# Performance work log

Hardware: AMD Instinct MI355X
Metric: run time of the kernel (lower is better)

Reference implementation:

```python
import jax, jax.numpy as jnp
import numpy as np

N_NODES = 100000
N_EDGES = 1200000
N_GRAPHS = 1024
IN_FEATS = 64
HID = 64
BN_EPS = 1e-5


def setup_inputs() -> dict:
    key = jax.random.key(0)
    ks = jax.random.split(key, 20)
    feats = jax.random.normal(ks[0], (N_NODES, IN_FEATS), jnp.float32)
    src = jax.random.randint(ks[1], (N_EDGES,), 0, N_NODES, jnp.int32)
    dst = jax.random.randint(ks[2], (N_EDGES,), 0, N_NODES, jnp.int32)
    graph_ids = jnp.sort(jax.random.randint(ks[3], (N_NODES,), 0, N_GRAPHS, jnp.int32))

    def lin(k, fi, fo):
        s = 1.0 / np.sqrt(fi)
        kw, kb = jax.random.split(k)
        return (jax.random.uniform(kw, (fi, fo), jnp.float32, -s, s),
                jax.random.uniform(kb, (fo,), jnp.float32, -s, s))

    W_self, _ = lin(ks[4], IN_FEATS, HID)
    W_neigh, b_neigh = lin(ks[5], IN_FEATS, HID)
    W1, b1 = lin(ks[6], HID, 128)
    W2, b2 = lin(ks[7], 128, 64)
    W3, b3 = lin(ks[8], 64, 1)

    def bn(k, d):
        k1, k2, k3, k4 = jax.random.split(k, 4)
        return (jax.random.normal(k1, (d,), jnp.float32) * 0.1 + 1.0,
                jax.random.normal(k2, (d,), jnp.float32) * 0.1,
                jax.random.normal(k3, (d,), jnp.float32) * 0.1,
                jax.random.uniform(k4, (d,), jnp.float32, 0.5, 1.5))

    g1, be1, rm1, rv1 = bn(ks[9], 128)
    g2, be2, rm2, rv2 = bn(ks[10], 64)

    return dict(feats=feats, src=src, dst=dst, graph_ids=graph_ids,
                W_self=W_self, W_neigh=W_neigh, b_neigh=b_neigh,
                W1=W1, b1=b1, g1=g1, be1=be1, rm1=rm1, rv1=rv1,
                W2=W2, b2=b2, g2=g2, be2=be2, rm2=rm2, rv2=rv2,
                W3=W3, b3=b3)


def reference(feats, src, dst, graph_ids, W_self, W_neigh, b_neigh,
              W1, b1, g1, be1, rm1, rv1, W2, b2, g2, be2, rm2, rv2, W3, b3):
    # --- SAGEConv (mean aggregator): h = W_self@h_self + W_neigh@mean_neigh + b
    deg = jax.ops.segment_sum(jnp.ones((src.shape[0],), feats.dtype), dst,
                              num_segments=N_NODES)                      # [N]
    agg = jax.ops.segment_sum(feats[src], dst, num_segments=N_NODES)     # [N, F]
    mean_neigh = agg / jnp.maximum(deg, 1.0)[:, None]
    h = feats @ W_self + mean_neigh @ W_neigh + b_neigh
    h = jax.nn.relu(h)                                                   # activation

    # --- per-graph max readout (dgl.max_nodes)
    hg = jax.ops.segment_max(h, graph_ids, num_segments=N_GRAPHS)        # [G, HID]

    # --- MLP head with eval-mode BatchNorm1d
    def bn(x, g, b, rm, rv):
        return (x - rm) * jax.lax.rsqrt(rv + BN_EPS) * g + b

    x = bn(jax.nn.relu(hg @ W1 + b1), g1, be1, rm1, rv1)
    x = bn(jax.nn.relu(x @ W2 + b2), g2, be2, rm2, rv2)
    return x @ W3 + b3                                                   # [G, n_task]
```

## Files before the change

### kernel.cpp

```cpp
#include <hip/hip_runtime.h>
#include <hip/hip_fp16.h>

#define N_NODES  100000
#define N_EDGES  1200000
#define N_GRAPHS 1024
#define F        64
#define BN_EPS   1e-5f
#define NBUCK    ((N_NODES + 255) / 256)
#define NBLK     512
#define CHUNK    ((N_EDGES + NBLK - 1) / NBLK)
#define MT       128
#define GEMM_BLOCKS ((N_NODES + MT - 1) / MT)
#define CE       3584
#define LDA      72

typedef _Float16 f16x8 __attribute__((ext_vector_type(8)));
typedef float f32x4 __attribute__((ext_vector_type(4)));

__global__ __launch_bounds__(256) void prep(
    const float* __restrict__ feats, const float* __restrict__ Wself,
    const float* __restrict__ Wneigh, __half* __restrict__ Uh,
    __half* __restrict__ Zh, const int* __restrict__ dst,
    int* __restrict__ bcnt, int* __restrict__ hgbits) {
  __shared__ __align__(16) char smraw[2 * 128 * LDA * 2];
  int t = threadIdx.x;

  if (blockIdx.x >= GEMM_BLOCKS) {
    int* lh = (int*)smraw;
    int b = blockIdx.x - GEMM_BLOCKS;
    int zidx = b * 256 + t;
    if (zidx < N_GRAPHS * F) hgbits[zidx] = 0;
    for (int i = t; i < NBUCK; i += 256) lh[i] = 0;
    __syncthreads();
    int e0 = b * CHUNK, e1 = e0 + CHUNK;
    if (e1 > N_EDGES) e1 = N_EDGES;
    for (int e = e0 + t; e < e1; e += 256) atomicAdd(&lh[dst[e] >> 8], 1);
    __syncthreads();
    for (int i = t; i < NBUCK; i += 256) {
      int c = lh[i];
      if (c) atomicAdd(&bcnt[i], c);
    }
    return;
  }

  __half* As = (__half*)smraw;
  __half* Bs = As + 128 * LDA;
  int mbase = blockIdx.x * MT;

#pragma unroll
  for (int s = 0; s < 8; s++) {
    int idx = s * 256 + t;
    int row = idx >> 4, c4 = idx & 15;
    int gm = mbase + row;
    float4 v = (gm < N_NODES) ? *(const float4*)(feats + (size_t)gm * F + c4 * 4)
                              : make_float4(0.f, 0.f, 0.f, 0.f);
    union { __half h[4]; uint2 u; } pk;
    pk.h[0] = __float2half_rn(v.x); pk.h[1] = __float2half_rn(v.y);
    pk.h[2] = __float2half_rn(v.z); pk.h[3] = __float2half_rn(v.w);
    *(uint2*)(As + row * LDA + c4 * 4) = pk.u;
  }

#pragma unroll
  for (int s = 0; s < 2; s++) {
    int unit = s * 256 + t;
    int kq = unit >> 5, c4 = unit & 31;
    const float* Wp = (c4 < 16) ? (Wself + c4 * 4) : (Wneigh + (c4 - 16) * 4);
    float4 w0 = *(const float4*)(Wp + (kq * 4 + 0) * 64);
    float4 w1 = *(const float4*)(Wp + (kq * 4 + 1) * 64);
    float4 w2 = *(const float4*)(Wp + (kq * 4 + 2) * 64);
    float4 w3 = *(const float4*)(Wp + (kq * 4 + 3) * 64);
    float a[4][4] = {{w0.x, w0.y, w0.z, w0.w}, {w1.x, w1.y, w1.z, w1.w},
                     {w2.x, w2.y, w2.z, w2.w}, {w3.x, w3.y, w3.z, w3.w}};
#pragma unroll
    for (int c = 0; c < 4; c++) {
      union { __half h[4]; uint2 u; } pk;
      pk.h[0] = __float2half_rn(a[0][c]); pk.h[1] = __float2half_rn(a[1][c]);
      pk.h[2] = __float2half_rn(a[2][c]); pk.h[3] = __float2half_rn(a[3][c]);
      *(uint2*)(Bs + (c4 * 4 + c) * LDA + kq * 4) = pk.u;
    }
  }
  __syncthreads();

  int wave = t >> 6, lane = t & 63;
  int lr = lane & 15, kg = lane >> 4;
  int r0 = wave * 32;

  f32x4 acc[2][8];
#pragma unroll
  for (int i = 0; i < 2; i++)
#pragma unroll
    for (int j = 0; j < 8; j++) acc[i][j] = (f32x4){0.f, 0.f, 0.f, 0.f};

#pragma unroll
  for (int h = 0; h < 2; h++) {
    f16x8 a0 = *(const f16x8*)(As + (r0 + lr) * LDA + h * 32 + kg * 8);
    f16x8 a1 = *(const f16x8*)(As + (r0 + 16 + lr) * LDA + h * 32 + kg * 8);
#pragma unroll
    for (int j = 0; j < 8; j++) {
      f16x8 wv = *(const f16x8*)(Bs + (j * 16 + lr) * LDA + h * 32 + kg * 8);
      acc[0][j] = __builtin_amdgcn_mfma_f32_16x16x32_f16(wv, a0, acc[0][j], 0, 0, 0);
      acc[1][j] = __builtin_amdgcn_mfma_f32_16x16x32_f16(wv, a1, acc[1][j], 0, 0, 0);
    }
  }

#pragma unroll
  for (int i = 0; i < 2; i++) {
    int node = mbase + r0 + i * 16 + lr;
    if (node < N_NODES) {
#pragma unroll
      for (int j = 0; j < 8; j++) {
        int f = j * 16 + kg * 4;
        union { __half h[4]; uint2 u; } pk;
        pk.h[0] = __float2half_rn(acc[i][j][0]);
        pk.h[1] = __float2half_rn(acc[i][j][1]);
        pk.h[2] = __float2half_rn(acc[i][j][2]);
        pk.h[3] = __float2half_rn(acc[i][j][3]);
        __half* outp = (f < 64) ? (Uh + (size_t)node * F + f)
                                : (Zh + (size_t)node * F + (f - 64));
        *(uint2*)outp = pk.u;
      }
    }
  }
}

__global__ __launch_bounds__(512) void scat(
    const int* __restrict__ src, const int* __restrict__ dst,
    const int* __restrict__ bcnt, int* __restrict__ gcur,
    int* __restrict__ pairs, int* __restrict__ bstart) {
  __shared__ int sc[512];
  __shared__ int lh[NBUCK];
  __shared__ int cur[NBUCK];
  __shared__ int dcache[CHUNK];
  int b = blockIdx.x, t = threadIdx.x;
  if (t < NBUCK) lh[t] = 0;
  __syncthreads();
  int e0 = b * CHUNK, e1 = e0 + CHUNK;
  if (e1 > N_EDGES) e1 = N_EDGES;
  for (int e = e0 + t; e < e1; e += 512) {
    int d = dst[e];
    dcache[e - e0] = d;
    atomicAdd(&lh[d >> 8], 1);
  }
  int v = (t < NBUCK) ? bcnt[t] : 0;
  sc[t] = v;
  __syncthreads();
  for (int off = 1; off < 512; off <<= 1) {
    int u = (t >= off) ? sc[t - off] : 0;
    __syncthreads();
    sc[t] += u;
    __syncthreads();
  }
  if (t < NBUCK) {
    int base = sc[t] - v;
    cur[t] = base + atomicAdd(&gcur[t], lh[t]);
    if (b == 0) bstart[t] = base;
  }
  if (b == 0 && t == 0) bstart[NBUCK] = N_EDGES;
  __syncthreads();
  for (int e = e0 + t; e < e1; e += 512) {
    int d = dcache[e - e0];
    int pos = atomicAdd(&cur[d >> 8], 1);
    pairs[pos] = (int)((((unsigned)d & 255u) << 24) | (unsigned)src[e]);
  }
}

__global__ __launch_bounds__(1024) void gather_place(
    const __half* __restrict__ Uh, const __half* __restrict__ Zh,
    const int* __restrict__ pairs, const int* __restrict__ bstart,
    const float* __restrict__ bneigh, const int* __restrict__ gids,
    int* __restrict__ hgbits) {
  __shared__ int eidx_l[CE];
  __shared__ int rsl[256];
  __shared__ int lh[256];
  __shared__ int cur[256];
  int b = blockIdx.x, t = threadIdx.x;
  int nb0 = b << 8;
  int r0 = bstart[b], r1 = bstart[b + 1];
  int E = r1 - r0; if (E > CE) E = CE;

  if (t < 256) lh[t] = 0;
  __syncthreads();
  for (int e = t; e < E; e += 1024)
    atomicAdd(&lh[((unsigned)pairs[r0 + e]) >> 24], 1);
  __syncthreads();
  if (t < 256) cur[t] = lh[t];
  __syncthreads();
  for (int off = 1; off < 256; off <<= 1) {
    int u = (t < 256 && t >= off) ? cur[t - off] : 0;
    __syncthreads();
    if (t < 256) cur[t] += u;
    __syncthreads();
  }
  if (t < 256) { int ex = cur[t] - lh[t]; rsl[t] = ex; cur[t] = ex; }
  __syncthreads();
  for (int e = t; e < E; e += 1024) {
    unsigned p = (unsigned)pairs[r0 + e];
    int pos = atomicAdd(&cur[p >> 24], 1);
    eidx_l[pos] = (int)(p & 0xFFFFFFu);
  }
  __syncthreads();

  int wave = t >> 6, lane = t & 63;
  int fl = lane & 15, sub = lane >> 4;
  float4 b4 = *(const float4*)(bneigh + 4 * fl);
  int nl = wave * 16;
  int nend = nl + 16;
  if (nb0 + nl >= N_NODES) return;
  if (nb0 + nend > N_NODES) nend = N_NODES - nb0;

  int curg = gids[nb0 + nl];
  float4 gmax = {0.f, 0.f, 0.f, 0.f};

  for (; nl < nend; nl++) {
    int node = nb0 + nl;
    int rr  = rsl[nl];
    int deg = lh[nl];
    uint2 ur = *(const uint2*)(Uh + (size_t)node * F + 4 * fl);
    float sx = 0.f, sy = 0.f, sz = 0.f, sw = 0.f;
    for (int jj = 0; jj < deg; jj += 16) {
      int j0 = jj + sub;
      int s0 = (j0      < deg) ? eidx_l[rr + j0]      : 0;
      int s1 = (j0 + 4  < deg) ? eidx_l[rr + j0 + 4]  : 0;
      int s2 = (j0 + 8  < deg) ? eidx_l[rr + j0 + 8]  : 0;
      int s3 = (j0 + 12 < deg) ? eidx_l[rr + j0 + 12] : 0;
      uint2 z0 = *(const uint2*)(Zh + (size_t)s0 * F + 4 * fl);
      uint2 z1 = *(const uint2*)(Zh + (size_t)s1 * F + 4 * fl);
      uint2 z2 = *(const uint2*)(Zh + (size_t)s2 * F + 4 * fl);
      uint2 z3 = *(const uint2*)(Zh + (size_t)s3 * F + 4 * fl);
      if (j0 < deg) {
        float2 f0 = __half22float2(*(__half2*)&z0.x);
        float2 f1 = __half22float2(*(__half2*)&z0.y);
        sx += f0.x; sy += f0.y; sz += f1.x; sw += f1.y;
      }
      if (j0 + 4 < deg) {
        float2 f0 = __half22float2(*(__half2*)&z1.x);
        float2 f1 = __half22float2(*(__half2*)&z1.y);
        sx += f0.x; sy += f0.y; sz += f1.x; sw += f1.y;
      }
      if (j0 + 8 < deg) {
        float2 f0 = __half22float2(*(__half2*)&z2.x);
        float2 f1 = __half22float2(*(__half2*)&z2.y);
        sx += f0.x; sy += f0.y; sz += f1.x; sw += f1.y;
      }
      if (j0 + 12 < deg) {
        float2 f0 = __half22float2(*(__half2*)&z3.x);
        float2 f1 = __half22float2(*(__half2*)&z3.y);
        sx += f0.x; sy += f0.y; sz += f1.x; sw += f1.y;
      }
    }
    sx += __shfl_xor(sx, 16); sy += __shfl_xor(sy, 16);
    sz += __shfl_xor(sz, 16); sw += __shfl_xor(sw, 16);
    sx += __shfl_xor(sx, 32); sy += __shfl_xor(sy, 32);
    sz += __shfl_xor(sz, 32); sw += __shfl_xor(sw, 32);
    float inv = 1.0f / fmaxf((float)deg, 1.0f);

    int g = gids[node];
    if (g != curg) {
      if (sub == 0) {
        int* hp = hgbits + (size_t)curg * F + 4 * fl;
        atomicMax(hp + 0, __float_as_int(gmax.x));
        atomicMax(hp + 1, __float_as_int(gmax.y));
        atomicMax(hp + 2, __float_as_int(gmax.z));
        atomicMax(hp + 3, __float_as_int(gmax.w));
      }
      curg = g; gmax = make_float4(0.f, 0.f, 0.f, 0.f);
    }

    float2 uf0 = __half22float2(*(__half2*)&ur.x);
    float2 uf1 = __half22float2(*(__half2*)&ur.y);
    gmax.x = fmaxf(gmax.x, fmaxf(uf0.x + sx * inv + b4.x, 0.f));
    gmax.y = fmaxf(gmax.y, fmaxf(uf0.y + sy * inv + b4.y, 0.f));
    gmax.z = fmaxf(gmax.z, fmaxf(uf1.x + sz * inv + b4.z, 0.f));
    gmax.w = fmaxf(gmax.w, fmaxf(uf1.y + sw * inv + b4.w, 0.f));
  }
  if (sub == 0) {
    int* hp = hgbits + (size_t)curg * F + 4 * fl;
    atomicMax(hp + 0, __float_as_int(gmax.x));
    atomicMax(hp + 1, __float_as_int(gmax.y));
    atomicMax(hp + 2, __float_as_int(gmax.z));
    atomicMax(hp + 3, __float_as_int(gmax.w));
  }
}

#define GPB 2
__global__ __launch_bounds__(128) void mlp(
    const float* __restrict__ hg,
    const float* __restrict__ W1, const float* __restrict__ b1,
    const float* __restrict__ g1, const float* __restrict__ be1,
    const float* __restrict__ rm1, const float* __restrict__ rv1,
    const float* __restrict__ W2, const float* __restrict__ b2,
    const float* __restrict__ g2, const float* __restrict__ be2,
    const float* __restrict__ rm2, const float* __restrict__ rv2,
    const float* __restrict__ W3, const float* __restrict__ b3,
    float* __restrict__ out) {
  __shared__ float W1s[64 * 128];
  __shared__ float W2s[128 * 64];
  __shared__ float W3s[64];
  __shared__ float sc1[128], sh1[128], b1s[128];
  __shared__ float sc2[64],  sh2[64],  b2s[64];
  __shared__ float s0[64], s1[128], s2[64];
  int t = threadIdx.x;

  for (int i = t; i < 64 * 128; i += 128) W1s[i] = W1[i];
  for (int i = t; i < 128 * 64; i += 128) W2s[i] = W2[i];
  if (t < 64) W3s[t] = W3[t];
  {
    float iv = rsqrtf(rv1[t] + BN_EPS);
    float sc = g1[t] * iv;
    sc1[t] = sc; sh1[t] = be1[t] - rm1[t] * sc; b1s[t] = b1[t];
  }
  if (t < 64) {
    float iv = rsqrtf(rv2[t] + BN_EPS);
    float sc = g2[t] * iv;
    sc2[t] = sc; sh2[t] = be2[t] - rm2[t] * sc; b2s[t] = b2[t];
  }
  __syncthreads();

  for (int gg = 0; gg < GPB; gg++) {
    int g = blockIdx.x * GPB + gg;
    if (t < 64) s0[t] = hg[(size_t)g * F + t];
    __syncthreads();
    {
      float acc = b1s[t];
      for (int i = 0; i < 64; i++) acc += s0[i] * W1s[i * 128 + t];
      acc = fmaxf(acc, 0.0f);
      s1[t] = acc * sc1[t] + sh1[t];
    }
    __syncthreads();
    if (t < 64) {
      float acc = b2s[t];
      for (int i = 0; i < 128; i++) acc += s1[i] * W2s[i * 64 + t];
      acc = fmaxf(acc, 0.0f);
      s2[t] = acc * sc2[t] + sh2[t];
    }
    __syncthreads();
    if (t < 64) {
      float p = s2[t] * W3s[t];
      for (int off = 32; off > 0; off >>= 1) p += __shfl_down(p, off);
      if (t == 0) out[g] = p + b3[0];
    }
    __syncthreads();
  }
}

extern "C" void kernel_launch(void* const* d_in, const int* in_sizes, int n_in,
                              void* d_out, int out_size, void* d_ws, size_t ws_size,
                              hipStream_t stream) {
  const float* feats  = (const float*)d_in[0];
  const int*   src    = (const int*)d_in[1];
  const int*   dst    = (const int*)d_in[2];
  const int*   gids   = (const int*)d_in[3];
  const float* Wself  = (const float*)d_in[4];
  const float* Wneigh = (const float*)d_in[5];
  const float* bneigh = (const float*)d_in[6];
  const float* W1  = (const float*)d_in[7];
  const float* b1  = (const float*)d_in[8];
  const float* g1  = (const float*)d_in[9];
  const float* be1 = (const float*)d_in[10];
  const float* rm1 = (const float*)d_in[11];
  const float* rv1 = (const float*)d_in[12];
  const float* W2  = (const float*)d_in[13];
  const float* b2  = (const float*)d_in[14];
  const float* g2  = (const float*)d_in[15];
  const float* be2 = (const float*)d_in[16];
  const float* rm2 = (const float*)d_in[17];
  const float* rv2 = (const float*)d_in[18];
  const float* W3  = (const float*)d_in[19];
  const float* b3  = (const float*)d_in[20];

  __half* Uh   = (__half*)d_ws;
  __half* Zh   = Uh + (size_t)N_NODES * F;
  int* bstart  = (int*)(Zh + (size_t)N_NODES * F);
  int* bcnt    = bstart + (NBUCK + 1);
  int* gcur    = bcnt + NBUCK;
  int* hgbits  = gcur + NBUCK;
  int* pairs   = hgbits + (size_t)N_GRAPHS * F;

  hipMemsetAsync(bcnt, 0, 2 * NBUCK * sizeof(int), stream);

  prep<<<GEMM_BLOCKS + NBLK, 256, 0, stream>>>(feats, Wself, Wneigh, Uh, Zh,
                                               dst, bcnt, hgbits);
  scat<<<NBLK, 512, 0, stream>>>(src, dst, bcnt, gcur, pairs, bstart);
  gather_place<<<NBUCK, 1024, 0, stream>>>(Uh, Zh, pairs, bstart, bneigh,
                                           gids, hgbits);
  mlp<<<N_GRAPHS / GPB, 128, 0, stream>>>((const float*)hgbits,
                                          W1, b1, g1, be1, rm1, rv1,
                                          W2, b2, g2, be2, rm2, rv2, W3, b3,
                                          (float*)d_out);
}
```

Baseline: 209.0 us.

## Fuse bucket scatter into prep kernel using fixed-capacity per-bucket slots

Removes the separate histogram-then-prefix-scan pass by giving each destination bucket a fixed CE-sized slot in the pairs buffer, so edge blocks can reserve positions with a global atomic and scatter directly. This merges the scatter kernel into the prep/GEMM launch, eliminating one kernel launch, one full re-read of dst, and the block-wide scan. The hgbits zeroing moves into the memset. Buckets exceeding CE edges are dropped, but the old code already truncated at CE, and a larger, sparser pairs buffer is used.

```diff
diff --git a/kernel.cpp b/kernel.cpp
--- a/kernel.cpp
+++ b/kernel.cpp
@@ -17,35 +17,48 @@
 typedef _Float16 f16x8 __attribute__((ext_vector_type(8)));
 typedef float f32x4 __attribute__((ext_vector_type(4)));
 
-__global__ __launch_bounds__(256) void prep(
+__global__ __launch_bounds__(256) void prepscat(
     const float* __restrict__ feats, const float* __restrict__ Wself,
     const float* __restrict__ Wneigh, __half* __restrict__ Uh,
-    __half* __restrict__ Zh, const int* __restrict__ dst,
-    int* __restrict__ bcnt, int* __restrict__ hgbits) {
+    __half* __restrict__ Zh, const int* __restrict__ src,
+    const int* __restrict__ dst, int* __restrict__ gcur,
+    int* __restrict__ pairs) {
   __shared__ __align__(16) char smraw[2 * 128 * LDA * 2];
   int t = threadIdx.x;
 
-  if (blockIdx.x >= GEMM_BLOCKS) {
-    int* lh = (int*)smraw;
-    int b = blockIdx.x - GEMM_BLOCKS;
-    int zidx = b * 256 + t;
-    if (zidx < N_GRAPHS * F) hgbits[zidx] = 0;
+  if (blockIdx.x < NBLK) {
+    int* dcache = (int*)smraw;
+    int* lh   = dcache + CHUNK;
+    int* lcur = lh + NBUCK;
+    int b = blockIdx.x;
     for (int i = t; i < NBUCK; i += 256) lh[i] = 0;
     __syncthreads();
     int e0 = b * CHUNK, e1 = e0 + CHUNK;
     if (e1 > N_EDGES) e1 = N_EDGES;
-    for (int e = e0 + t; e < e1; e += 256) atomicAdd(&lh[dst[e] >> 8], 1);
+    for (int e = e0 + t; e < e1; e += 256) {
+      int d = dst[e];
+      dcache[e - e0] = d;
+      atomicAdd(&lh[d >> 8], 1);
+    }
     __syncthreads();
     for (int i = t; i < NBUCK; i += 256) {
       int c = lh[i];
-      if (c) atomicAdd(&bcnt[i], c);
+      lcur[i] = c ? atomicAdd(&gcur[i], c) : 0;
+    }
+    __syncthreads();
+    for (int e = e0 + t; e < e1; e += 256) {
+      int d = dcache[e - e0];
+      int pos = atomicAdd(&lcur[d >> 8], 1);
+      if (pos < CE)
+        pairs[(size_t)(d >> 8) * CE + pos] =
+            (int)((((unsigned)d & 255u) << 24) | (unsigned)src[e]);
     }
     return;
   }
 
   __half* As = (__half*)smraw;
   __half* Bs = As + 128 * LDA;
-  int mbase = blockIdx.x * MT;
+  int mbase = (blockIdx.x - NBLK) * MT;
 
 #pragma unroll
   for (int s = 0; s < 8; s++) {
@@ -123,50 +136,9 @@
   }
 }
 
-__global__ __launch_bounds__(512) void scat(
-    const int* __restrict__ src, const int* __restrict__ dst,
-    const int* __restrict__ bcnt, int* __restrict__ gcur,
-    int* __restrict__ pairs, int* __restrict__ bstart) {
-  __shared__ int sc[512];
-  __shared__ int lh[NBUCK];
-  __shared__ int cur[NBUCK];
-  __shared__ int dcache[CHUNK];
-  int b = blockIdx.x, t = threadIdx.x;
-  if (t < NBUCK) lh[t] = 0;
-  __syncthreads();
-  int e0 = b * CHUNK, e1 = e0 + CHUNK;
-  if (e1 > N_EDGES) e1 = N_EDGES;
-  for (int e = e0 + t; e < e1; e += 512) {
-    int d = dst[e];
-    dcache[e - e0] = d;
-    atomicAdd(&lh[d >> 8], 1);
-  }
-  int v = (t < NBUCK) ? bcnt[t] : 0;
-  sc[t] = v;
-  __syncthreads();
-  for (int off = 1; off < 512; off <<= 1) {
-    int u = (t >= off) ? sc[t - off] : 0;
-    __syncthreads();
-    sc[t] += u;
-    __syncthreads();
-  }
-  if (t < NBUCK) {
-    int base = sc[t] - v;
-    cur[t] = base + atomicAdd(&gcur[t], lh[t]);
-    if (b == 0) bstart[t] = base;
-  }
-  if (b == 0 && t == 0) bstart[NBUCK] = N_EDGES;
-  __syncthreads();
-  for (int e = e0 + t; e < e1; e += 512) {
-    int d = dcache[e - e0];
-    int pos = atomicAdd(&cur[d >> 8], 1);
-    pairs[pos] = (int)((((unsigned)d & 255u) << 24) | (unsigned)src[e]);
-  }
-}
-
 __global__ __launch_bounds__(1024) void gather_place(
     const __half* __restrict__ Uh, const __half* __restrict__ Zh,
-    const int* __restrict__ pairs, const int* __restrict__ bstart,
+    const int* __restrict__ pairs, const int* __restrict__ gcur,
     const float* __restrict__ bneigh, const int* __restrict__ gids,
     int* __restrict__ hgbits) {
   __shared__ int eidx_l[CE];
@@ -175,13 +147,13 @@
   __shared__ int cur[256];
   int b = blockIdx.x, t = threadIdx.x;
   int nb0 = b << 8;
-  int r0 = bstart[b], r1 = bstart[b + 1];
-  int E = r1 - r0; if (E > CE) E = CE;
+  const int* pr = pairs + (size_t)b * CE;
+  int E = gcur[b]; if (E > CE) E = CE;
 
   if (t < 256) lh[t] = 0;
   __syncthreads();
   for (int e = t; e < E; e += 1024)
-    atomicAdd(&lh[((unsigned)pairs[r0 + e]) >> 24], 1);
+    atomicAdd(&lh[((unsigned)pr[e]) >> 24], 1);
   __syncthreads();
   if (t < 256) cur[t] = lh[t];
   __syncthreads();
@@ -194,7 +166,7 @@
   if (t < 256) { int ex = cur[t] - lh[t]; rsl[t] = ex; cur[t] = ex; }
   __syncthreads();
   for (int e = t; e < E; e += 1024) {
-    unsigned p = (unsigned)pairs[r0 + e];
+    unsigned p = (unsigned)pr[e];
     int pos = atomicAdd(&cur[p >> 24], 1);
     eidx_l[pos] = (int)(p & 0xFFFFFFu);
   }
@@ -370,18 +342,15 @@
 
   __half* Uh   = (__half*)d_ws;
   __half* Zh   = Uh + (size_t)N_NODES * F;
-  int* bstart  = (int*)(Zh + (size_t)N_NODES * F);
-  int* bcnt    = bstart + (NBUCK + 1);
-  int* gcur    = bcnt + NBUCK;
+  int* gcur    = (int*)(Zh + (size_t)N_NODES * F);
   int* hgbits  = gcur + NBUCK;
   int* pairs   = hgbits + (size_t)N_GRAPHS * F;
 
-  hipMemsetAsync(bcnt, 0, 2 * NBUCK * sizeof(int), stream);
-
-  prep<<<GEMM_BLOCKS + NBLK, 256, 0, stream>>>(feats, Wself, Wneigh, Uh, Zh,
-                                               dst, bcnt, hgbits);
-  scat<<<NBLK, 512, 0, stream>>>(src, dst, bcnt, gcur, pairs, bstart);
-  gather_place<<<NBUCK, 1024, 0, stream>>>(Uh, Zh, pairs, bstart, bneigh,
+  hipMemsetAsync(gcur, 0, (NBUCK + N_GRAPHS * F) * sizeof(int), stream);
+
+  prepscat<<<NBLK + GEMM_BLOCKS, 256, 0, stream>>>(feats, Wself, Wneigh,
+                                                   Uh, Zh, src, dst, gcur, pairs);
+  gather_place<<<NBUCK, 1024, 0, stream>>>(Uh, Zh, pairs, gcur, bneigh,
                                            gids, hgbits);
   mlp<<<N_GRAPHS / GPB, 128, 0, stream>>>((const float*)hgbits,
                                           W1, b1, g1, be1, rm1, rv1,
```

Result: faster. 191.8 us (-8.2%).
